# Kernel optimization log

Measured on AMD Instinct MI355X. Metric: run time of the kernel, lower is better.

The kernel has to match this reference:

```python
import jax, jax.numpy as jnp
import numpy as np

B = 64          # graphs per batch
NPG = 4000      # nodes per graph
CPG0 = 400      # level-0 clusters per graph
CPG1 = 40       # level-1 clusters per graph
DEG = 8         # avg degree
F_IN = 64       # node feature dim (input_shape)


def setup_inputs() -> dict:
    rng = np.random.RandomState(0)
    N0 = B * NPG
    E0 = N0 * DEG
    N1 = B * CPG0
    N2 = B * CPG1
    # node -> graph and node -> level-0 cluster (globally consecutive ids)
    node_graph = np.repeat(np.arange(N0 // NPG), NPG)
    local = np.tile(np.arange(NPG), B)
    cluster0 = node_graph * CPG0 + local // (NPG // CPG0)
    # random edges, endpoints within the same graph
    edge_graph = np.repeat(np.arange(B), NPG * DEG)
    src = edge_graph * NPG + rng.randint(0, NPG, size=E0)
    dst = edge_graph * NPG + rng.randint(0, NPG, size=E0)
    edge_index = np.stack([src, dst]).astype(np.int64)
    # community_pooling's pool_edge: map edges through cluster0, drop self-loops,
    # coalesce duplicates (edge_attr summed). Precompute the integer structure.
    ci, cj = cluster0[src], cluster0[dst]
    mask = ci != cj
    key_ = ci.astype(np.int64) * N1 + cj.astype(np.int64)
    uniq, inv = np.unique(key_[mask], return_inverse=True)
    E1 = uniq.shape[0]
    edge_seg = np.full(E0, E1, dtype=np.int64)   # dropped self-loops -> dummy seg E1
    edge_seg[mask] = inv
    edge_index1 = np.stack([uniq // N1, uniq % N1]).astype(np.int64)
    # level-1 clusters on pooled nodes and graph id of each level-1 cluster
    cl_idx = np.arange(N1)
    cluster1 = (cl_idx // CPG0) * CPG1 + (cl_idx % CPG0) // (CPG0 // CPG1)
    batch2 = np.arange(N2) // CPG1

    key = jax.random.key(0)
    ks = jax.random.split(key, 10)

    def lin(k, fin, fout):
        return jax.random.normal(k, (fin, fout), jnp.float32) / np.sqrt(fin)

    return dict(
        x=jax.random.normal(ks[0], (N0, F_IN), jnp.float32),
        edge_attr=jax.random.uniform(ks[1], (E0, 1), jnp.float32),
        edge_index=jnp.asarray(edge_index),
        cluster0=jnp.asarray(cluster0.astype(np.int64)),
        edge_index1=jnp.asarray(edge_index1),
        edge_seg=jnp.asarray(edge_seg),
        cluster1=jnp.asarray(cluster1.astype(np.int64)),
        batch2=jnp.asarray(batch2.astype(np.int64)),
        n_clusters0=N1, n_clusters1=N2, n_graphs=B,
        W1=lin(ks[2], F_IN, 16), We1=lin(ks[3], 1, 1), Wa1=lin(ks[4], 2 * 16 + 1, 1),
        W2=lin(ks[5], 16, 32), We2=lin(ks[6], 1, 1), Wa2=lin(ks[7], 2 * 32 + 1, 1),
        fc1_W=lin(ks[8], 32, 64), fc1_b=jnp.zeros((64,), jnp.float32),
        fc2_W=lin(ks[9], 64, 1), fc2_b=jnp.zeros((1,), jnp.float32),
    )


def _gin_conv(x, edge_index, edge_attr, W, We, Wa, num_nodes):
    # DeepRank-GNN GINetConvLayer (all linears bias-free)
    row, col = edge_index[0], edge_index[1]
    xp = x @ W                      # project once, then gather (same math as fc(x[col]))
    xrow, xcol = xp[row], xp[col]   # (E, out)
    ed = edge_attr @ We             # (E, n_edge_feat)
    alpha = jnp.concatenate([xrow, xcol, ed], axis=1) @ Wa   # (E, 1)
    alpha = jax.nn.leaky_relu(alpha)
    # faithful: softmax over dim=1 of an (E,1) tensor -> all ones
    alpha = jax.nn.softmax(alpha, axis=1)
    h = alpha * xcol
    return jax.ops.segment_sum(h, row, num_segments=num_nodes)


def reference(x, edge_attr, edge_index, cluster0, edge_index1, edge_seg,
              cluster1, batch2, n_clusters0, n_clusters1, n_graphs,
              W1, We1, Wa1, W2, We2, Wa2, fc1_W, fc1_b, fc2_W, fc2_b):
    # conv1 + relu
    x1 = jax.nn.relu(_gin_conv(x, edge_index, edge_attr, W1, We1, Wa1, x.shape[0]))
    # community_pooling: scatter_max nodes onto clusters, coalesced pooled edges
    x_pool = jax.ops.segment_max(x1, cluster0, num_segments=n_clusters0)
    E1 = edge_index1.shape[1]
    ea1 = jax.ops.segment_sum(edge_attr, edge_seg, num_segments=E1 + 1)[:E1]
    # conv2 + relu on pooled graph
    x2 = jax.nn.relu(_gin_conv(x_pool, edge_index1, ea1, W2, We2, Wa2, n_clusters0))
    # max_pool_x over level-1 clusters, then scatter_mean per graph
    x3 = jax.ops.segment_max(x2, cluster1, num_segments=n_clusters1)
    s = jax.ops.segment_sum(x3, batch2, num_segments=n_graphs)
    cnt = jax.ops.segment_sum(jnp.ones((x3.shape[0], 1), x3.dtype), batch2,
                              num_segments=n_graphs)
    xg = s / cnt                                  # (B, 32)
    h = jax.nn.relu(xg @ fc1_W + fc1_b)           # (B, 64)
    return h @ fc2_W + fc2_b                      # (B, 1)
```

## Files before the change

### kernel.cpp

```cpp
#include <hip/hip_runtime.h>
#include <hip/hip_bf16.h>


#define C1 16
#define C2 32
#define NPG 4000
#define EPG 32000
#define P   8
#define EPP (EPG / P)
#define RPB 80

__global__ void gemm1_k(const float* __restrict__ x, const float* __restrict__ W,
                        float* __restrict__ xp1, int N0) {
    int n = blockIdx.x * blockDim.x + threadIdx.x;
    if (n >= N0) return;
    const float4* xr = (const float4*)(x + (size_t)n * 64);
    float acc[C1];
#pragma unroll
    for (int j = 0; j < C1; ++j) acc[j] = 0.f;
#pragma unroll
    for (int k4 = 0; k4 < 16; ++k4) {
        float4 v = xr[k4];
        const float* w0 = W + (k4 * 4 + 0) * C1;
        const float* w1 = W + (k4 * 4 + 1) * C1;
        const float* w2 = W + (k4 * 4 + 2) * C1;
        const float* w3 = W + (k4 * 4 + 3) * C1;
#pragma unroll
        for (int j = 0; j < C1; ++j)
            acc[j] += v.x * w0[j] + v.y * w1[j] + v.z * w2[j] + v.w * w3[j];
    }
    float4* o = (float4*)(xp1 + (size_t)n * C1);
#pragma unroll
    for (int q = 0; q < 4; ++q)
        o[q] = make_float4(acc[4 * q], acc[4 * q + 1], acc[4 * q + 2], acc[4 * q + 3]);
}

__global__ __launch_bounds__(1024) void csr0_k(const int* __restrict__ ei,
                                               int* __restrict__ rp0,
                                               int* __restrict__ scol,
                                               int E0, int B) {
    __shared__ int cnt[NPG];
    __shared__ int tsum[1024];
    int g = blockIdx.x % B;
    int p = blockIdx.x / B;
    int t = threadIdx.x;
    const int* rows = ei + (size_t)g * EPG + p * EPP;
    const int* cols = ei + E0 + (size_t)g * EPG + p * EPP;
    int rbase = g * NPG;
    int ebase = g * EPG + p * EPP;
    int* rpp = rp0 + (size_t)(p * B + g) * (NPG + 1);

    for (int i = t; i < NPG; i += 1024) cnt[i] = 0;
    __syncthreads();
    for (int e = t; e < EPP; e += 1024) atomicAdd(&cnt[rows[e] - rbase], 1);
    __syncthreads();

    int loc[4];
    int s = 0;
#pragma unroll
    for (int k = 0; k < 4; ++k) {
        int idx = 4 * t + k;
        int v = (idx < NPG) ? cnt[idx] : 0;
        loc[k] = s;
        s += v;
    }
    tsum[t] = s;
    __syncthreads();
    int mine = s;
    for (int off = 1; off < 1024; off <<= 1) {
        int u = (t >= off) ? tsum[t - off] : 0;
        __syncthreads();
        tsum[t] += u;
        __syncthreads();
    }
    int excl = tsum[t] - mine;
#pragma unroll
    for (int k = 0; k < 4; ++k) {
        int idx = 4 * t + k;
        if (idx < NPG) {
            int pos = excl + loc[k];
            rpp[idx] = ebase + pos;
            cnt[idx] = pos;
        }
    }
    if (t == 1023) rpp[NPG] = ebase + EPP;
    __syncthreads();

    for (int e = t; e < EPP; e += 1024) {
        int r = rows[e] - rbase;
        int c = cols[e];
        int pos = atomicAdd(&cnt[r], 1);
        scol[ebase + pos] = c;
    }
}

__global__ __launch_bounds__(256) void merge_k(const int* __restrict__ rp0,
                                               const int* __restrict__ scol,
                                               int* __restrict__ rp2,
                                               int* __restrict__ scol2,
                                               int B, int N0, int E0) {
    int g = blockIdx.x % B;
    int cb = blockIdx.x / B;
    int t = threadIdx.x;
    if (blockIdx.x == 0 && t == 0) rp2[N0] = E0;
    int rl = cb * 256 + t;
    if (rl >= NPG) return;
    int r = g * NPG + rl;
    int s0[P], cnt[P];
    int sum = 0;
#pragma unroll
    for (int p = 0; p < P; ++p) {
        const int* rpp = rp0 + (size_t)(p * B + g) * (NPG + 1) + rl;
        int a = rpp[0];
        int b = rpp[1];
        s0[p] = a;
        cnt[p] = b - a;
        sum += a;
    }
    int base = sum - (P - 1) * g * EPG - EPP * (P * (P - 1) / 2);
    rp2[r] = base;
    int wpos[P];
    int w = base;
#pragma unroll
    for (int p = 0; p < P; ++p) { wpos[p] = w; w += cnt[p]; }
#pragma unroll
    for (int p = 0; p < P; ++p)
        if (cnt[p] > 0) scol2[wpos[p]] = scol[s0[p]];
#pragma unroll
    for (int p = 0; p < P; ++p)
        for (int k = 1; k < cnt[p]; ++k)
            scol2[wpos[p] + k] = scol[s0[p] + k];
}

__global__ __launch_bounds__(320) void aggell_k(const int* __restrict__ rp2,
                                                const int* __restrict__ scol2,
                                                const float* __restrict__ xp1,
                                                float* __restrict__ xpool,
                                                int B, int cpg) {
    __shared__ float4 sums[RPB][4];
    int g = blockIdx.x % B;
    int cb = blockIdx.x / B;
    int t = threadIdx.x;
    int f4 = t & 3;
    int rl = t >> 2;
    int r = g * NPG + cb * RPB + rl;
    int e0 = rp2[r];
    int cnt = rp2[r + 1] - e0;
    const float4* xp = (const float4*)xp1;
    float4 s = make_float4(0.f, 0.f, 0.f, 0.f);
#pragma unroll
    for (int k = 0; k < 16; ++k) {
        if (k < cnt) {
            float4 v = xp[(size_t)scol2[e0 + k] * 4 + f4];
            s.x += v.x; s.y += v.y; s.z += v.z; s.w += v.w;
        }
    }
    for (int k = 16; k < cnt; ++k) {
        float4 v = xp[(size_t)scol2[e0 + k] * 4 + f4];
        s.x += v.x; s.y += v.y; s.z += v.z; s.w += v.w;
    }
    sums[rl][f4] = s;
    __syncthreads();
    if (t < 32) {
        int cl = t >> 2, ff = t & 3;
        float4 m = sums[cl * 10][ff];
#pragma unroll
        for (int k = 1; k < 10; ++k) {
            float4 v = sums[cl * 10 + k][ff];
            m.x = fmaxf(m.x, v.x); m.y = fmaxf(m.y, v.y);
            m.z = fmaxf(m.z, v.z); m.w = fmaxf(m.w, v.w);
        }
        m.x = fmaxf(m.x, 0.f); m.y = fmaxf(m.y, 0.f);
        m.z = fmaxf(m.z, 0.f); m.w = fmaxf(m.w, 0.f);
        ((float4*)xpool)[(size_t)(g * cpg + cb * 8 + cl) * 4 + ff] = m;
    }
}

__global__ void gemm2_k(const float* __restrict__ xp, const float* __restrict__ W,
                        float* __restrict__ xp2, int N1) {
    int n = blockIdx.x * blockDim.x + threadIdx.x;
    if (n >= N1) return;
    const float4* xr = (const float4*)(xp + (size_t)n * C1);
    float acc[C2];
#pragma unroll
    for (int j = 0; j < C2; ++j) acc[j] = 0.f;
#pragma unroll
    for (int k4 = 0; k4 < 4; ++k4) {
        float4 v = xr[k4];
        const float* w0 = W + (k4 * 4 + 0) * C2;
        const float* w1 = W + (k4 * 4 + 1) * C2;
        const float* w2 = W + (k4 * 4 + 2) * C2;
        const float* w3 = W + (k4 * 4 + 3) * C2;
#pragma unroll
        for (int j = 0; j < C2; ++j)
            acc[j] += v.x * w0[j] + v.y * w1[j] + v.z * w2[j] + v.w * w3[j];
    }
    float4* o = (float4*)(xp2 + (size_t)n * C2);
#pragma unroll
    for (int q = 0; q < 8; ++q)
        o[q] = make_float4(acc[4 * q], acc[4 * q + 1], acc[4 * q + 2], acc[4 * q + 3]);
}

__global__ void rowptr_k(const int* __restrict__ ei1, int* __restrict__ rp, int E1, int N1) {
    int e = blockIdx.x * blockDim.x + threadIdx.x;
    if (e >= E1) return;
    int r = ei1[e];
    int rprev = __shfl_up(r, 1);
    if ((threadIdx.x & 63) == 0) rprev = (e == 0) ? -1 : ei1[e - 1];
    for (int rr = rprev + 1; rr <= r; ++rr) rp[rr] = e;
    if (e == E1 - 1)
        for (int rr = r + 1; rr <= N1; ++rr) rp[rr] = E1;
}

__global__ __launch_bounds__(256) void edge_agg2_k(const int* __restrict__ ei1,
                                                   const int* __restrict__ rp,
                                                   const float* __restrict__ xp2,
                                                   float* __restrict__ x2acc,
                                                   int E1, int B, int cpg) {
    int g = blockIdx.x % B;
    int c = blockIdx.x / B;
    int t = threadIdx.x;
    int f4 = t & 7;
    int es = (t >> 3) & 7;
    int r = g * cpg + c * 4 + (t >> 6);
    const int* col = ei1 + E1;
    float4 acc = make_float4(0.f, 0.f, 0.f, 0.f);
    int e0 = rp[r], e1 = rp[r + 1];
    for (int e = e0 + es; e < e1; e += 8) {
        const float4* src = (const float4*)(xp2 + (size_t)col[e] * C2);
        float4 v = src[f4];
        acc.x += v.x; acc.y += v.y; acc.z += v.z; acc.w += v.w;
    }
#pragma unroll
    for (int off = 8; off <= 32; off <<= 1) {
        acc.x += __shfl_xor(acc.x, off);
        acc.y += __shfl_xor(acc.y, off);
        acc.z += __shfl_xor(acc.z, off);
        acc.w += __shfl_xor(acc.w, off);
    }
    if (es == 0) ((float4*)(x2acc + (size_t)r * C2))[f4] = acc;
}

__global__ __launch_bounds__(256) void final_k(const float* __restrict__ x2acc,
                                               const float* __restrict__ fc1W,
                                               const float* __restrict__ fc1b,
                                               const float* __restrict__ fc2W,
                                               const float* __restrict__ fc2b,
                                               float* __restrict__ out, int cpg) {
    __shared__ float xgs[C2];
    int g = blockIdx.x;
    int t = threadIdx.x;
    if (t < C2) xgs[t] = 0.f;
    __syncthreads();
    for (int i = t; i < 40 * C2; i += 256) {
        int cl = i >> 5, f = i & 31;
        const float* base = x2acc + ((size_t)g * cpg + cl * 10) * C2 + f;
        float m = base[0];
#pragma unroll
        for (int k = 1; k < 10; ++k) m = fmaxf(m, base[k * C2]);
        atomicAdd(&xgs[f], fmaxf(m, 0.f));
    }
    __syncthreads();
    if (t < 64) {
        float h = fc1b[t];
#pragma unroll
        for (int f = 0; f < C2; ++f) h += xgs[f] * (1.f / 40.f) * fc1W[f * 64 + t];
        h = fmaxf(h, 0.f);
        float v = h * fc2W[t];
#pragma unroll
        for (int off = 32; off > 0; off >>= 1) v += __shfl_down(v, off);
        if (t == 0) out[g] = v + fc2b[0];
    }
}

extern "C" void kernel_launch(void* const* d_in, const int* in_sizes, int n_in,
                              void* d_out, int out_size, void* d_ws, size_t ws_size,
                              hipStream_t stream) {
    const float* x    = (const float*)d_in[0];
    const int*   ei   = (const int*)d_in[2];
    const int*   ei1  = (const int*)d_in[4];
    const float* W1   = (const float*)d_in[11];
    const float* W2   = (const float*)d_in[14];
    const float* fc1W = (const float*)d_in[17];
    const float* fc1b = (const float*)d_in[18];
    const float* fc2W = (const float*)d_in[19];
    const float* fc2b = (const float*)d_in[20];
    float* out = (float*)d_out;

    const int N0 = in_sizes[0] / 64;
    const int E0 = in_sizes[2] / 2;
    const int E1 = in_sizes[4] / 2;
    const int N1 = in_sizes[6];
    const int N2 = in_sizes[7];
    const int B  = N2 / 40;
    const int CPG0 = N1 / B;

    float* xp1   = (float*)d_ws;
    float* xpool = xp1 + (size_t)N0 * C1;
    float* xp2   = xpool + (size_t)N1 * C1;
    float* x2acc = xp2 + (size_t)N1 * C2;
    int*   rp1   = (int*)(x2acc + (size_t)N1 * C2);
    int*   rp0   = rp1 + (N1 + 2);
    int*   scol  = rp0 + (size_t)B * P * (NPG + 1) + 2;
    int*   scol2 = scol + (size_t)E0;
    int*   rp2   = scol2 + (size_t)E0;

    gemm1_k<<<(N0 + 255) / 256, 256, 0, stream>>>(x, W1, xp1, N0);
    csr0_k<<<B * P, 1024, 0, stream>>>(ei, rp0, scol, E0, B);
    merge_k<<<B * ((NPG + 255) / 256), 256, 0, stream>>>(rp0, scol, rp2, scol2, B, N0, E0);
    aggell_k<<<B * (NPG / RPB), 320, 0, stream>>>(rp2, scol2, xp1, xpool, B, CPG0);
    gemm2_k<<<(N1 + 255) / 256, 256, 0, stream>>>(xpool, W2, xp2, N1);
    rowptr_k<<<(E1 + 255) / 256, 256, 0, stream>>>(ei1, rp1, E1, N1);
    edge_agg2_k<<<B * (CPG0 / 4), 256, 0, stream>>>(ei1, rp1, xp2, x2acc, E1, B, CPG0);
    final_k<<<B, 256, 0, stream>>>(x2acc, fc1W, fc1b, fc2W, fc2b, out, CPG0);
}
```

Baseline: 266.6 us.

## Fuse conv2 GEMM, edge aggregation and level-1 max pooling into one kernel

Replaces the separate gemm2 and edge_agg2 kernels with a per-graph-quarter kernel. It computes the 400-row projected features of one graph into padded shared memory, gathers neighbours from LDS instead of global memory, and does the level-1 max pool and ReLU in the same kernel. The final kernel now only averages 40 pooled rows. This drops two launches and the global round trip of xp2 and x2acc, but each graph's GEMM is recomputed four times (once per block) and only 256 blocks are launched, with large LDS use.

```diff
diff --git a/kernel.cpp b/kernel.cpp
--- a/kernel.cpp
+++ b/kernel.cpp
@@ -9,6 +9,7 @@
 #define P   8
 #define EPP (EPG / P)
 #define RPB 80
+#define XSTR 36
 
 __global__ void gemm1_k(const float* __restrict__ x, const float* __restrict__ W,
                         float* __restrict__ xp1, int N0) {
@@ -174,31 +175,6 @@
         m.z = fmaxf(m.z, 0.f); m.w = fmaxf(m.w, 0.f);
         ((float4*)xpool)[(size_t)(g * cpg + cb * 8 + cl) * 4 + ff] = m;
     }
-}
-
-__global__ void gemm2_k(const float* __restrict__ xp, const float* __restrict__ W,
-                        float* __restrict__ xp2, int N1) {
-    int n = blockIdx.x * blockDim.x + threadIdx.x;
-    if (n >= N1) return;
-    const float4* xr = (const float4*)(xp + (size_t)n * C1);
-    float acc[C2];
-#pragma unroll
-    for (int j = 0; j < C2; ++j) acc[j] = 0.f;
-#pragma unroll
-    for (int k4 = 0; k4 < 4; ++k4) {
-        float4 v = xr[k4];
-        const float* w0 = W + (k4 * 4 + 0) * C2;
-        const float* w1 = W + (k4 * 4 + 1) * C2;
-        const float* w2 = W + (k4 * 4 + 2) * C2;
-        const float* w3 = W + (k4 * 4 + 3) * C2;
-#pragma unroll
-        for (int j = 0; j < C2; ++j)
-            acc[j] += v.x * w0[j] + v.y * w1[j] + v.z * w2[j] + v.w * w3[j];
-    }
-    float4* o = (float4*)(xp2 + (size_t)n * C2);
-#pragma unroll
-    for (int q = 0; q < 8; ++q)
-        o[q] = make_float4(acc[4 * q], acc[4 * q + 1], acc[4 * q + 2], acc[4 * q + 3]);
 }
 
 __global__ void rowptr_k(const int* __restrict__ ei1, int* __restrict__ rp, int E1, int N1) {
@@ -212,65 +188,99 @@
         for (int rr = r + 1; rr <= N1; ++rr) rp[rr] = E1;
 }
 
-__global__ __launch_bounds__(256) void edge_agg2_k(const int* __restrict__ ei1,
-                                                   const int* __restrict__ rp,
-                                                   const float* __restrict__ xp2,
-                                                   float* __restrict__ x2acc,
-                                                   int E1, int B, int cpg) {
+__global__ __launch_bounds__(256) void conv2_k(const float* __restrict__ xpool,
+                                               const float* __restrict__ W,
+                                               const int* __restrict__ ei1,
+                                               const int* __restrict__ rp,
+                                               float* __restrict__ x3,
+                                               int E1, int B, int cpg) {
+    __shared__ __align__(16) float xp2s[400 * XSTR];
+    __shared__ __align__(16) float res[100 * C2];
     int g = blockIdx.x % B;
-    int c = blockIdx.x / B;
-    int t = threadIdx.x;
+    int q = blockIdx.x / B;
+    int t = threadIdx.x;
+
+    for (int r = t; r < 400; r += 256) {
+        const float4* xr = (const float4*)(xpool + (size_t)(g * cpg + r) * C1);
+        float acc[C2];
+#pragma unroll
+        for (int j = 0; j < C2; ++j) acc[j] = 0.f;
+#pragma unroll
+        for (int k4 = 0; k4 < 4; ++k4) {
+            float4 v = xr[k4];
+            const float* w0 = W + (k4 * 4 + 0) * C2;
+            const float* w1 = W + (k4 * 4 + 1) * C2;
+            const float* w2 = W + (k4 * 4 + 2) * C2;
+            const float* w3 = W + (k4 * 4 + 3) * C2;
+#pragma unroll
+            for (int j = 0; j < C2; ++j)
+                acc[j] += v.x * w0[j] + v.y * w1[j] + v.z * w2[j] + v.w * w3[j];
+        }
+        float4* o = (float4*)(xp2s + r * XSTR);
+#pragma unroll
+        for (int j4 = 0; j4 < 8; ++j4)
+            o[j4] = make_float4(acc[4 * j4], acc[4 * j4 + 1], acc[4 * j4 + 2], acc[4 * j4 + 3]);
+    }
+    __syncthreads();
+
     int f4 = t & 7;
     int es = (t >> 3) & 7;
-    int r = g * cpg + c * 4 + (t >> 6);
+    int w = t >> 6;
     const int* col = ei1 + E1;
-    float4 acc = make_float4(0.f, 0.f, 0.f, 0.f);
-    int e0 = rp[r], e1 = rp[r + 1];
-    for (int e = e0 + es; e < e1; e += 8) {
-        const float4* src = (const float4*)(xp2 + (size_t)col[e] * C2);
-        float4 v = src[f4];
-        acc.x += v.x; acc.y += v.y; acc.z += v.z; acc.w += v.w;
-    }
-#pragma unroll
-    for (int off = 8; off <= 32; off <<= 1) {
-        acc.x += __shfl_xor(acc.x, off);
-        acc.y += __shfl_xor(acc.y, off);
-        acc.z += __shfl_xor(acc.z, off);
-        acc.w += __shfl_xor(acc.w, off);
-    }
-    if (es == 0) ((float4*)(x2acc + (size_t)r * C2))[f4] = acc;
-}
-
-__global__ __launch_bounds__(256) void final_k(const float* __restrict__ x2acc,
-                                               const float* __restrict__ fc1W,
-                                               const float* __restrict__ fc1b,
-                                               const float* __restrict__ fc2W,
-                                               const float* __restrict__ fc2b,
-                                               float* __restrict__ out, int cpg) {
-    __shared__ float xgs[C2];
+    for (int i = 0; i < 25; ++i) {
+        int rloc = w * 25 + i;
+        int rg = g * cpg + q * 100 + rloc;
+        float4 acc = make_float4(0.f, 0.f, 0.f, 0.f);
+        int e0 = rp[rg], e1e = rp[rg + 1];
+        for (int e = e0 + es; e < e1e; e += 8) {
+            int lc = col[e] - g * cpg;
+            float4 v = ((const float4*)(xp2s + lc * XSTR))[f4];
+            acc.x += v.x; acc.y += v.y; acc.z += v.z; acc.w += v.w;
+        }
+#pragma unroll
+        for (int off = 8; off <= 32; off <<= 1) {
+            acc.x += __shfl_xor(acc.x, off);
+            acc.y += __shfl_xor(acc.y, off);
+            acc.z += __shfl_xor(acc.z, off);
+            acc.w += __shfl_xor(acc.w, off);
+        }
+        if (es == 0) ((float4*)(res + rloc * C2))[f4] = acc;
+    }
+    __syncthreads();
+
+    for (int i = t; i < 10 * C2; i += 256) {
+        int cl = i >> 5, f = i & 31;
+        float m = res[(cl * 10) * C2 + f];
+#pragma unroll
+        for (int k = 1; k < 10; ++k) m = fmaxf(m, res[(cl * 10 + k) * C2 + f]);
+        x3[((size_t)g * 40 + q * 10 + cl) * C2 + f] = fmaxf(m, 0.f);
+    }
+}
+
+__global__ __launch_bounds__(64) void final_k(const float* __restrict__ x3,
+                                              const float* __restrict__ fc1W,
+                                              const float* __restrict__ fc1b,
+                                              const float* __restrict__ fc2W,
+                                              const float* __restrict__ fc2b,
+                                              float* __restrict__ out) {
+    __shared__ float xg[C2];
     int g = blockIdx.x;
     int t = threadIdx.x;
-    if (t < C2) xgs[t] = 0.f;
-    __syncthreads();
-    for (int i = t; i < 40 * C2; i += 256) {
-        int cl = i >> 5, f = i & 31;
-        const float* base = x2acc + ((size_t)g * cpg + cl * 10) * C2 + f;
-        float m = base[0];
-#pragma unroll
-        for (int k = 1; k < 10; ++k) m = fmaxf(m, base[k * C2]);
-        atomicAdd(&xgs[f], fmaxf(m, 0.f));
-    }
-    __syncthreads();
-    if (t < 64) {
-        float h = fc1b[t];
-#pragma unroll
-        for (int f = 0; f < C2; ++f) h += xgs[f] * (1.f / 40.f) * fc1W[f * 64 + t];
-        h = fmaxf(h, 0.f);
-        float v = h * fc2W[t];
-#pragma unroll
-        for (int off = 32; off > 0; off >>= 1) v += __shfl_down(v, off);
-        if (t == 0) out[g] = v + fc2b[0];
-    }
+    if (t < C2) {
+        float s = 0.f;
+        const float* base = x3 + (size_t)g * 40 * C2 + t;
+        for (int r = 0; r < 40; ++r) s += base[r * C2];
+        xg[t] = s * (1.f / 40.f);
+    }
+    __syncthreads();
+    float h = fc1b[t];
+#pragma unroll
+    for (int f = 0; f < C2; ++f) h += xg[f] * fc1W[f * 64 + t];
+    h = fmaxf(h, 0.f);
+    float v = h * fc2W[t];
+#pragma unroll
+    for (int off = 32; off > 0; off >>= 1) v += __shfl_down(v, off);
+    if (t == 0) out[g] = v + fc2b[0];
 }
 
 extern "C" void kernel_launch(void* const* d_in, const int* in_sizes, int n_in,
@@ -297,9 +307,8 @@
 
     float* xp1   = (float*)d_ws;
     float* xpool = xp1 + (size_t)N0 * C1;
-    float* xp2   = xpool + (size_t)N1 * C1;
-    float* x2acc = xp2 + (size_t)N1 * C2;
-    int*   rp1   = (int*)(x2acc + (size_t)N1 * C2);
+    float* x3    = xpool + (size_t)N1 * C1;
+    int*   rp1   = (int*)(x3 + (size_t)N2 * C2);
     int*   rp0   = rp1 + (N1 + 2);
     int*   scol  = rp0 + (size_t)B * P * (NPG + 1) + 2;
     int*   scol2 = scol + (size_t)E0;
@@ -309,8 +318,7 @@
     csr0_k<<<B * P, 1024, 0, stream>>>(ei, rp0, scol, E0, B);
     merge_k<<<B * ((NPG + 255) / 256), 256, 0, stream>>>(rp0, scol, rp2, scol2, B, N0, E0);
     aggell_k<<<B * (NPG / RPB), 320, 0, stream>>>(rp2, scol2, xp1, xpool, B, CPG0);
-    gemm2_k<<<(N1 + 255) / 256, 256, 0, stream>>>(xpool, W2, xp2, N1);
     rowptr_k<<<(E1 + 255) / 256, 256, 0, stream>>>(ei1, rp1, E1, N1);
-    edge_agg2_k<<<B * (CPG0 / 4), 256, 0, stream>>>(ei1, rp1, xp2, x2acc, E1, B, CPG0);
-    final_k<<<B, 256, 0, stream>>>(x2acc, fc1W, fc1b, fc2W, fc2b, out, CPG0);
-}
+    conv2_k<<<B * 4, 256, 0, stream>>>(xpool, W2, ei1, rp1, x3, E1, B, CPG0);
+    final_k<<<B, 64, 0, stream>>>(x3, fc1W, fc1b, fc2W, fc2b, out);
+}
```

After: 322.1 us. 1.21x slower.

## Aggregate pooled features before applying W2 and fuse gemm2 into edge aggregation

Applied to the files above, without the earlier changes.

The second GIN layer now sums the 16-wide pooled neighbour features per cluster first and applies the 16x32 W2 weight afterwards, instead of projecting every cluster to 32 features and then aggregating. This relies on linearity to remove the separate gemm2 kernel launch and the xp2 intermediate buffer, and it halves the bytes gathered per edge. In exchange, each block does a small shared-memory matvec after a barrier, and fp32 summation order shifts slightly.

```diff
diff --git a/kernel.cpp b/kernel.cpp
--- a/kernel.cpp
+++ b/kernel.cpp
@@ -174,31 +174,6 @@
         m.z = fmaxf(m.z, 0.f); m.w = fmaxf(m.w, 0.f);
         ((float4*)xpool)[(size_t)(g * cpg + cb * 8 + cl) * 4 + ff] = m;
     }
-}
-
-__global__ void gemm2_k(const float* __restrict__ xp, const float* __restrict__ W,
-                        float* __restrict__ xp2, int N1) {
-    int n = blockIdx.x * blockDim.x + threadIdx.x;
-    if (n >= N1) return;
-    const float4* xr = (const float4*)(xp + (size_t)n * C1);
-    float acc[C2];
-#pragma unroll
-    for (int j = 0; j < C2; ++j) acc[j] = 0.f;
-#pragma unroll
-    for (int k4 = 0; k4 < 4; ++k4) {
-        float4 v = xr[k4];
-        const float* w0 = W + (k4 * 4 + 0) * C2;
-        const float* w1 = W + (k4 * 4 + 1) * C2;
-        const float* w2 = W + (k4 * 4 + 2) * C2;
-        const float* w3 = W + (k4 * 4 + 3) * C2;
-#pragma unroll
-        for (int j = 0; j < C2; ++j)
-            acc[j] += v.x * w0[j] + v.y * w1[j] + v.z * w2[j] + v.w * w3[j];
-    }
-    float4* o = (float4*)(xp2 + (size_t)n * C2);
-#pragma unroll
-    for (int q = 0; q < 8; ++q)
-        o[q] = make_float4(acc[4 * q], acc[4 * q + 1], acc[4 * q + 2], acc[4 * q + 3]);
 }
 
 __global__ void rowptr_k(const int* __restrict__ ei1, int* __restrict__ rp, int E1, int N1) {
@@ -212,33 +187,49 @@
         for (int rr = r + 1; rr <= N1; ++rr) rp[rr] = E1;
 }
 
-__global__ __launch_bounds__(256) void edge_agg2_k(const int* __restrict__ ei1,
-                                                   const int* __restrict__ rp,
-                                                   const float* __restrict__ xp2,
-                                                   float* __restrict__ x2acc,
-                                                   int E1, int B, int cpg) {
+__global__ __launch_bounds__(256) void agg2_k(const int* __restrict__ ei1,
+                                              const int* __restrict__ rp,
+                                              const float* __restrict__ xpool,
+                                              const float* __restrict__ W2,
+                                              float* __restrict__ x2acc,
+                                              int E1, int B, int cpg) {
+    __shared__ float sums[4][C1];
     int g = blockIdx.x % B;
     int c = blockIdx.x / B;
     int t = threadIdx.x;
-    int f4 = t & 7;
-    int es = (t >> 3) & 7;
-    int r = g * cpg + c * 4 + (t >> 6);
+    int f4 = t & 3;
+    int es = (t >> 2) & 15;
+    int w = t >> 6;
+    int r = g * cpg + c * 4 + w;
     const int* col = ei1 + E1;
     float4 acc = make_float4(0.f, 0.f, 0.f, 0.f);
-    int e0 = rp[r], e1 = rp[r + 1];
-    for (int e = e0 + es; e < e1; e += 8) {
-        const float4* src = (const float4*)(xp2 + (size_t)col[e] * C2);
-        float4 v = src[f4];
+    int e0 = rp[r], e1e = rp[r + 1];
+    for (int e = e0 + es; e < e1e; e += 16) {
+        float4 v = ((const float4*)(xpool + (size_t)col[e] * C1))[f4];
         acc.x += v.x; acc.y += v.y; acc.z += v.z; acc.w += v.w;
     }
 #pragma unroll
-    for (int off = 8; off <= 32; off <<= 1) {
+    for (int off = 4; off <= 32; off <<= 1) {
         acc.x += __shfl_xor(acc.x, off);
         acc.y += __shfl_xor(acc.y, off);
         acc.z += __shfl_xor(acc.z, off);
         acc.w += __shfl_xor(acc.w, off);
     }
-    if (es == 0) ((float4*)(x2acc + (size_t)r * C2))[f4] = acc;
+    if (es == 0) {
+        sums[w][f4 * 4 + 0] = acc.x;
+        sums[w][f4 * 4 + 1] = acc.y;
+        sums[w][f4 * 4 + 2] = acc.z;
+        sums[w][f4 * 4 + 3] = acc.w;
+    }
+    __syncthreads();
+    if (t < 128) {
+        int w2 = t >> 5, j = t & 31;
+        const float* s = sums[w2];
+        float v = 0.f;
+#pragma unroll
+        for (int k = 0; k < C1; ++k) v += s[k] * W2[k * C2 + j];
+        x2acc[(size_t)(g * cpg + c * 4 + w2) * C2 + j] = v;
+    }
 }
 
 __global__ __launch_bounds__(256) void final_k(const float* __restrict__ x2acc,
@@ -297,8 +288,7 @@
 
     float* xp1   = (float*)d_ws;
     float* xpool = xp1 + (size_t)N0 * C1;
-    float* xp2   = xpool + (size_t)N1 * C1;
-    float* x2acc = xp2 + (size_t)N1 * C2;
+    float* x2acc = xpool + (size_t)N1 * C1;
     int*   rp1   = (int*)(x2acc + (size_t)N1 * C2);
     int*   rp0   = rp1 + (N1 + 2);
     int*   scol  = rp0 + (size_t)B * P * (NPG + 1) + 2;
@@ -309,8 +299,7 @@
     csr0_k<<<B * P, 1024, 0, stream>>>(ei, rp0, scol, E0, B);
     merge_k<<<B * ((NPG + 255) / 256), 256, 0, stream>>>(rp0, scol, rp2, scol2, B, N0, E0);
     aggell_k<<<B * (NPG / RPB), 320, 0, stream>>>(rp2, scol2, xp1, xpool, B, CPG0);
-    gemm2_k<<<(N1 + 255) / 256, 256, 0, stream>>>(xpool, W2, xp2, N1);
     rowptr_k<<<(E1 + 255) / 256, 256, 0, stream>>>(ei1, rp1, E1, N1);
-    edge_agg2_k<<<B * (CPG0 / 4), 256, 0, stream>>>(ei1, rp1, xp2, x2acc, E1, B, CPG0);
+    agg2_k<<<B * (CPG0 / 4), 256, 0, stream>>>(ei1, rp1, xpool, W2, x2acc, E1, B, CPG0);
     final_k<<<B, 256, 0, stream>>>(x2acc, fc1W, fc1b, fc2W, fc2b, out, CPG0);
 }
```

New measurement: 257.4 us. 3.4% less time.
